# Kernel optimization log

Measured on AMD Instinct MI355X. Metric: run time of the kernel, lower is better.

The kernel has to match this reference:

```python
import jax, jax.numpy as jnp
import numpy as np

NUM_VARI = 32
DIM_PER_VARI = 128  # input feature dim is 2*DIM_PER_VARI
DIM_TO = 256
BATCH = 4096
TWO_D = 2 * DIM_PER_VARI


def setup_inputs() -> dict:
    key = jax.random.key(0)
    k1, k2, k3 = jax.random.split(key, 3)
    x = jax.random.normal(k1, (NUM_VARI, BATCH, TWO_D), dtype=jnp.float32)
    # parameters, initialized like reset_parameters(): U(-std, std), std = 1/sqrt(num_vari)
    std = 1.0 / np.sqrt(NUM_VARI)
    dense_w = jax.random.uniform(k2, (NUM_VARI, 1, TWO_D, DIM_TO), dtype=jnp.float32,
                                 minval=-std, maxval=std)
    dense_bias = jax.random.uniform(k3, (NUM_VARI, 1, 1, DIM_TO), dtype=jnp.float32,
                                    minval=-std, maxval=std)
    return {"x": x, "dense_w": dense_w, "dense_bias": dense_bias}


def reference(x, dense_w, dense_bias):
    # Original: (x.unsqueeze(-1) * W + b).sum(2)
    # = grouped matmul over the feature axis + (2*dim_per_vari) * bias
    # x: [V, B, 2D], W: [V, 1, 2D, O] -> out: [V, B, O]
    out = jnp.einsum('vbd,vdo->vbo', x, dense_w[:, 0])
    out = out + TWO_D * dense_bias[:, 0]  # bias broadcast [V,1,O] -> [V,B,O]
    # activation_type == 'softplus' (original intends F.softplus)
    return jax.nn.softplus(out)
```

## Files before the change

### kernel.cpp

```cpp
#include <hip/hip_runtime.h>
#include <stdint.h>
#include <math.h>

#define NV 32
#define NB 4096
#define NK 256
#define NO 256

#define TROWS 16
#define NTILE 16

typedef __bf16 bf16x8 __attribute__((ext_vector_type(8)));
typedef float  f32x4  __attribute__((ext_vector_type(4)));

__device__ __forceinline__ f32x4 mfma16(bf16x8 a, bf16x8 b, f32x4 c) {
    return __builtin_amdgcn_mfma_f32_16x16x32_bf16(a, b, c, 0, 0, 0);
}

__device__ __forceinline__ float softplus_f(float z) {
    return fmaxf(z, 0.0f) + __logf(1.0f + __expf(-fabsf(z)));
}

__device__ __forceinline__ void gload_lds16(const void* g, void* l) {
    __builtin_amdgcn_global_load_lds((const __attribute__((address_space(1))) uint32_t*)g,
                                     (__attribute__((address_space(3))) uint32_t*)l,
                                     16, 0, 0);
}

__global__ __launch_bounds__(256)
void prep_wt_kernel(const float* __restrict__ w, __bf16* __restrict__ wt) {
    const int id = blockIdx.x * 256 + threadIdx.x;
    const int o  = id & 255;
    const int kc = (id >> 8) & 31;
    const int v  = id >> 13;
    const float* src = w + ((size_t)v * NK + (size_t)kc * 8) * NO + o;
    bf16x8 r;
#pragma unroll
    for (int j = 0; j < 8; ++j) r[j] = (__bf16)src[(size_t)j * NO];
    *(bf16x8*)(wt + ((size_t)v * NO + o) * NK + kc * 8) = r;
}

__global__ __launch_bounds__(512, 4)
void mv_dense_kernel(const float* __restrict__ x, const __bf16* __restrict__ wt,
                     const float* __restrict__ bias, float* __restrict__ out) {
    __shared__ float Xs[3][TROWS][NK];

    const int t    = threadIdx.x;
    const int w    = t >> 6;
    const int lane = t & 63;
    const int lr   = lane & 15;
    const int lg   = lane >> 4;

    const int bid  = blockIdx.x;
    const int lb   = (bid & 7) * 64 + (bid >> 3);
    const int v    = lb >> 4;
    const int slab = lb & 15;

    const float*  xg = x    + ((size_t)v * NB + (size_t)slab * 256) * NK;
    float*        og = out  + ((size_t)v * NB + (size_t)slab * 256) * NO;

    const __bf16* wp0 = wt + ((size_t)v * NO + w * 32 + lr) * NK + lg * 8;
    const __bf16* wp1 = wp0 + (size_t)16 * NK;
    bf16x8 wv0[8], wv1[8];
#pragma unroll
    for (int kk = 0; kk < 8; ++kk) {
        wv0[kk] = *(const bf16x8*)(wp0 + kk * 32);
        wv1[kk] = *(const bf16x8*)(wp1 + kk * 32);
    }

    const float* bg = bias + (size_t)v * NO + w * 32 + lg * 4;
    f32x4 bb0 = *(const f32x4*)bg;
    f32x4 bb1 = *(const f32x4*)(bg + 16);
#pragma unroll
    for (int r = 0; r < 4; ++r) { bb0[r] *= 256.0f; bb1[r] *= 256.0f; }

    const int cl = lane ^ (w & 7);
    auto stage = [&](int tile, int buf) {
        const float* s0 = xg + (size_t)(tile * TROWS + w)     * NK + cl * 4;
        const float* s1 = xg + (size_t)(tile * TROWS + w + 8) * NK + cl * 4;
        gload_lds16(s0, (void*)&Xs[buf][w][0]);
        gload_lds16(s1, (void*)&Xs[buf][w + 8][0]);
    };

    const int b0c   = (2 * lg) ^ (lr & 7);
    const int aoff0 = lr * 1024 + b0c * 16;
    const int aoff1 = lr * 1024 + (b0c ^ 1) * 16;

    auto compute = [&](int tile, int buf) {
        const char* tb = (const char*)&Xs[buf][0][0];
        f32x4 acc0 = {0.f, 0.f, 0.f, 0.f};
        f32x4 acc1 = {0.f, 0.f, 0.f, 0.f};
#pragma unroll
        for (int kk = 0; kk < 8; ++kk) {
            f32x4 lo = *(const f32x4*)(tb + aoff0 + kk * 128);
            f32x4 hi = *(const f32x4*)(tb + aoff1 + kk * 128);
            bf16x8 bf;
#pragma unroll
            for (int e = 0; e < 4; ++e) { bf[e] = (__bf16)lo[e]; bf[e + 4] = (__bf16)hi[e]; }
            acc0 = mfma16(wv0[kk], bf, acc0);
            acc1 = mfma16(wv1[kk], bf, acc1);
        }
        float* o = og + (size_t)(tile * TROWS + lr) * NO + w * 32 + lg * 4;
        f32x4 r0, r1;
#pragma unroll
        for (int r = 0; r < 4; ++r) {
            r0[r] = softplus_f(acc0[r] + bb0[r]);
            r1[r] = softplus_f(acc1[r] + bb1[r]);
        }
        *(f32x4*)o        = r0;
        *(f32x4*)(o + 16) = r1;
    };

    stage(0, 0);
    stage(1, 1);

    asm volatile("s_waitcnt vmcnt(0)" ::: "memory");
    __builtin_amdgcn_s_barrier();
    __builtin_amdgcn_sched_barrier(0);
    stage(2, 2);
    compute(0, 0);

#pragma unroll 1
    for (int tt = 1; tt < NTILE; ++tt) {
        asm volatile("s_waitcnt vmcnt(4)" ::: "memory");
        __builtin_amdgcn_s_barrier();
        __builtin_amdgcn_sched_barrier(0);
        if (tt + 2 < NTILE) stage(tt + 2, (tt + 2) % 3);
        compute(tt, tt % 3);
    }
}

extern "C" void kernel_launch(void* const* d_in, const int* in_sizes, int n_in,
                              void* d_out, int out_size, void* d_ws, size_t ws_size,
                              hipStream_t stream) {
    const float* x  = (const float*)d_in[0];
    const float* w  = (const float*)d_in[1];
    const float* b  = (const float*)d_in[2];
    float* out      = (float*)d_out;
    __bf16* wt      = (__bf16*)d_ws;

    hipLaunchKernelGGL(prep_wt_kernel, dim3(1024), dim3(256), 0, stream, w, wt);
    hipLaunchKernelGGL(mv_dense_kernel, dim3(512), dim3(512), 0, stream,
                       x, wt, b, out);
}
```

Measured before the change: 66.38 us.

## Stage x through registers as bf16 in LDS with larger 64-row tiles

The x tile is no longer copied into LDS as fp32 by direct global-to-LDS loads. Instead it is loaded into registers, converted to bf16, and written into a swizzled, double-buffered LDS tile of 64 rows rather than 16. Each wave now computes four 16-row MFMA blocks per tile, and the weight fragments are re-read from global memory inside the k loop instead of being kept in registers. The aim is to halve LDS footprint and traffic, convert each x element once, and cut the number of barriers. In exchange it adds repeated weight loads, register-staged prefetch and a shallower pipeline.

```diff
diff --git a/kernel.cpp b/kernel.cpp
--- a/kernel.cpp
+++ b/kernel.cpp
@@ -7,10 +7,11 @@
 #define NK 256
 #define NO 256
 
-#define TROWS 16
-#define NTILE 16
+#define TROWS 64
+#define NTILE 4
 
 typedef __bf16 bf16x8 __attribute__((ext_vector_type(8)));
+typedef __bf16 bf16x4 __attribute__((ext_vector_type(4)));
 typedef float  f32x4  __attribute__((ext_vector_type(4)));
 
 __device__ __forceinline__ f32x4 mfma16(bf16x8 a, bf16x8 b, f32x4 c) {
@@ -19,12 +20,6 @@
 
 __device__ __forceinline__ float softplus_f(float z) {
     return fmaxf(z, 0.0f) + __logf(1.0f + __expf(-fabsf(z)));
-}
-
-__device__ __forceinline__ void gload_lds16(const void* g, void* l) {
-    __builtin_amdgcn_global_load_lds((const __attribute__((address_space(1))) uint32_t*)g,
-                                     (__attribute__((address_space(3))) uint32_t*)l,
-                                     16, 0, 0);
 }
 
 __global__ __launch_bounds__(256)
@@ -43,7 +38,7 @@
 __global__ __launch_bounds__(512, 4)
 void mv_dense_kernel(const float* __restrict__ x, const __bf16* __restrict__ wt,
                      const float* __restrict__ bias, float* __restrict__ out) {
-    __shared__ float Xs[3][TROWS][NK];
+    __shared__ __bf16 Xs[2][TROWS * NK];
 
     const int t    = threadIdx.x;
     const int w    = t >> 6;
@@ -56,17 +51,11 @@
     const int v    = lb >> 4;
     const int slab = lb & 15;
 
-    const float*  xg = x    + ((size_t)v * NB + (size_t)slab * 256) * NK;
-    float*        og = out  + ((size_t)v * NB + (size_t)slab * 256) * NO;
+    const float* xg = x   + ((size_t)v * NB + (size_t)slab * 256) * NK;
+    float*       og = out + ((size_t)v * NB + (size_t)slab * 256) * NO;
 
     const __bf16* wp0 = wt + ((size_t)v * NO + w * 32 + lr) * NK + lg * 8;
     const __bf16* wp1 = wp0 + (size_t)16 * NK;
-    bf16x8 wv0[8], wv1[8];
-#pragma unroll
-    for (int kk = 0; kk < 8; ++kk) {
-        wv0[kk] = *(const bf16x8*)(wp0 + kk * 32);
-        wv1[kk] = *(const bf16x8*)(wp1 + kk * 32);
-    }
 
     const float* bg = bias + (size_t)v * NO + w * 32 + lg * 4;
     f32x4 bb0 = *(const f32x4*)bg;
@@ -74,59 +63,81 @@
 #pragma unroll
     for (int r = 0; r < 4; ++r) { bb0[r] *= 256.0f; bb1[r] *= 256.0f; }
 
-    const int cl = lane ^ (w & 7);
-    auto stage = [&](int tile, int buf) {
-        const float* s0 = xg + (size_t)(tile * TROWS + w)     * NK + cl * 4;
-        const float* s1 = xg + (size_t)(tile * TROWS + w + 8) * NK + cl * 4;
-        gload_lds16(s0, (void*)&Xs[buf][w][0]);
-        gload_lds16(s1, (void*)&Xs[buf][w + 8][0]);
+    const float* xsrc = xg + w * NK + lane * 4;
+    const int ldso = w * NK + (((lane >> 1) ^ w) * 8) + (lane & 1) * 4;
+
+    f32x4 xa[8];
+    auto stage_load = [&](int tile) {
+#pragma unroll
+        for (int n = 0; n < 8; ++n)
+            xa[n] = *(const f32x4*)(xsrc + (size_t)tile * TROWS * NK + n * 8 * NK);
+    };
+    auto cvt_write = [&](__bf16* buf) {
+#pragma unroll
+        for (int n = 0; n < 8; ++n) {
+            bf16x4 hv;
+#pragma unroll
+            for (int e = 0; e < 4; ++e) hv[e] = (__bf16)xa[n][e];
+            *(bf16x4*)&buf[n * 8 * NK + ldso] = hv;
+        }
     };
 
-    const int b0c   = (2 * lg) ^ (lr & 7);
-    const int aoff0 = lr * 1024 + b0c * 16;
-    const int aoff1 = lr * 1024 + (b0c ^ 1) * 16;
-
-    auto compute = [&](int tile, int buf) {
-        const char* tb = (const char*)&Xs[buf][0][0];
-        f32x4 acc0 = {0.f, 0.f, 0.f, 0.f};
-        f32x4 acc1 = {0.f, 0.f, 0.f, 0.f};
+    auto compute = [&](int tile, const __bf16* buf) {
+        f32x4 acc[4][2];
+#pragma unroll
+        for (int i = 0; i < 4; ++i)
+#pragma unroll
+            for (int j = 0; j < 2; ++j) {
+                f32x4 z4 = {0.f, 0.f, 0.f, 0.f};
+                acc[i][j] = z4;
+            }
 #pragma unroll
         for (int kk = 0; kk < 8; ++kk) {
-            f32x4 lo = *(const f32x4*)(tb + aoff0 + kk * 128);
-            f32x4 hi = *(const f32x4*)(tb + aoff1 + kk * 128);
-            bf16x8 bf;
+            bf16x8 wv0 = *(const bf16x8*)(wp0 + kk * 32);
+            bf16x8 wv1 = *(const bf16x8*)(wp1 + kk * 32);
 #pragma unroll
-            for (int e = 0; e < 4; ++e) { bf[e] = (__bf16)lo[e]; bf[e + 4] = (__bf16)hi[e]; }
-            acc0 = mfma16(wv0[kk], bf, acc0);
-            acc1 = mfma16(wv1[kk], bf, acc1);
+            for (int i = 0; i < 4; ++i) {
+                const int row  = i * 16 + lr;
+                const int phys = (kk * 4 + lg) ^ (lr & 7);
+                bf16x8 afr = *(const bf16x8*)&buf[row * NK + phys * 8];
+                acc[i][0] = mfma16(wv0, afr, acc[i][0]);
+                acc[i][1] = mfma16(wv1, afr, acc[i][1]);
+            }
         }
-        float* o = og + (size_t)(tile * TROWS + lr) * NO + w * 32 + lg * 4;
-        f32x4 r0, r1;
 #pragma unroll
-        for (int r = 0; r < 4; ++r) {
-            r0[r] = softplus_f(acc0[r] + bb0[r]);
-            r1[r] = softplus_f(acc1[r] + bb1[r]);
+        for (int i = 0; i < 4; ++i) {
+            float* o = og + (size_t)(tile * TROWS + i * 16 + lr) * NO + w * 32 + lg * 4;
+            f32x4 r0, r1;
+#pragma unroll
+            for (int r = 0; r < 4; ++r) {
+                r0[r] = softplus_f(acc[i][0][r] + bb0[r]);
+                r1[r] = softplus_f(acc[i][1][r] + bb1[r]);
+            }
+            *(f32x4*)o        = r0;
+            *(f32x4*)(o + 16) = r1;
         }
-        *(f32x4*)o        = r0;
-        *(f32x4*)(o + 16) = r1;
     };
 
-    stage(0, 0);
-    stage(1, 1);
+    stage_load(0);
+    asm volatile("s_waitcnt vmcnt(0)" ::: "memory");
+    cvt_write(&Xs[0][0]);
+    stage_load(1);
+    __builtin_amdgcn_sched_barrier(0);
+    __builtin_amdgcn_s_barrier();
 
-    asm volatile("s_waitcnt vmcnt(0)" ::: "memory");
-    __builtin_amdgcn_s_barrier();
-    __builtin_amdgcn_sched_barrier(0);
-    stage(2, 2);
-    compute(0, 0);
-
+    __bf16* cur = &Xs[0][0];
+    __bf16* nxt = &Xs[1][0];
 #pragma unroll 1
-    for (int tt = 1; tt < NTILE; ++tt) {
-        asm volatile("s_waitcnt vmcnt(4)" ::: "memory");
-        __builtin_amdgcn_s_barrier();
-        __builtin_amdgcn_sched_barrier(0);
-        if (tt + 2 < NTILE) stage(tt + 2, (tt + 2) % 3);
-        compute(tt, tt % 3);
+    for (int tt = 0; tt < NTILE; ++tt) {
+        compute(tt, cur);
+        if (tt + 1 < NTILE) {
+            asm volatile("s_waitcnt vmcnt(8)" ::: "memory");
+            cvt_write(nxt);
+            if (tt + 2 < NTILE) stage_load(tt + 2);
+            __builtin_amdgcn_sched_barrier(0);
+            __builtin_amdgcn_s_barrier();
+            __bf16* tmp = cur; cur = nxt; nxt = tmp;
+        }
     }
 }
 
```

After: 112.9 us. 70.1% more time.

## Halve rows per block, double grid, and reload weights per tile instead of registers

Applied to the files above, without the earlier changes.

Each block now handles 128 batch rows (8 tiles) instead of 256, and the grid grows to 1024 blocks to spread work over more CUs and waves. The bf16 weight fragments are no longer held in 32 registers across the loop but reloaded from global/L2 inside each k step, which lowers register pressure. Occupancy hint drops from 4 to 3 and the LDS swizzle is rewritten per row. In exchange, weight loads repeat every tile and the shorter per-block pipeline exposes more prologue/epilogue overhead.

```diff
diff --git a/kernel.cpp b/kernel.cpp
--- a/kernel.cpp
+++ b/kernel.cpp
@@ -8,7 +8,7 @@
 #define NO 256
 
 #define TROWS 16
-#define NTILE 16
+#define NTILE 8
 
 typedef __bf16 bf16x8 __attribute__((ext_vector_type(8)));
 typedef float  f32x4  __attribute__((ext_vector_type(4)));
@@ -40,10 +40,10 @@
     *(bf16x8*)(wt + ((size_t)v * NO + o) * NK + kc * 8) = r;
 }
 
-__global__ __launch_bounds__(512, 4)
+__global__ __launch_bounds__(512, 3)
 void mv_dense_kernel(const float* __restrict__ x, const __bf16* __restrict__ wt,
                      const float* __restrict__ bias, float* __restrict__ out) {
-    __shared__ float Xs[3][TROWS][NK];
+    __shared__ float Xs[3][TROWS * NK];
 
     const int t    = threadIdx.x;
     const int w    = t >> 6;
@@ -52,21 +52,15 @@
     const int lg   = lane >> 4;
 
     const int bid  = blockIdx.x;
-    const int lb   = (bid & 7) * 64 + (bid >> 3);
-    const int v    = lb >> 4;
-    const int slab = lb & 15;
+    const int lb   = (bid & 7) * 128 + (bid >> 3);
+    const int v    = lb >> 5;
+    const int slab = lb & 31;
 
-    const float*  xg = x    + ((size_t)v * NB + (size_t)slab * 256) * NK;
-    float*        og = out  + ((size_t)v * NB + (size_t)slab * 256) * NO;
+    const float* xg = x   + ((size_t)v * NB + (size_t)slab * 128) * NK;
+    float*       og = out + ((size_t)v * NB + (size_t)slab * 128) * NO;
 
     const __bf16* wp0 = wt + ((size_t)v * NO + w * 32 + lr) * NK + lg * 8;
     const __bf16* wp1 = wp0 + (size_t)16 * NK;
-    bf16x8 wv0[8], wv1[8];
-#pragma unroll
-    for (int kk = 0; kk < 8; ++kk) {
-        wv0[kk] = *(const bf16x8*)(wp0 + kk * 32);
-        wv1[kk] = *(const bf16x8*)(wp1 + kk * 32);
-    }
 
     const float* bg = bias + (size_t)v * NO + w * 32 + lg * 4;
     f32x4 bb0 = *(const f32x4*)bg;
@@ -74,33 +68,35 @@
 #pragma unroll
     for (int r = 0; r < 4; ++r) { bb0[r] *= 256.0f; bb1[r] *= 256.0f; }
 
-    const int cl = lane ^ (w & 7);
     auto stage = [&](int tile, int buf) {
-        const float* s0 = xg + (size_t)(tile * TROWS + w)     * NK + cl * 4;
-        const float* s1 = xg + (size_t)(tile * TROWS + w + 8) * NK + cl * 4;
-        gload_lds16(s0, (void*)&Xs[buf][w][0]);
-        gload_lds16(s1, (void*)&Xs[buf][w + 8][0]);
+        const float* tsrc = xg + (size_t)tile * TROWS * NK;
+        char* lbase = (char*)&Xs[buf][0];
+#pragma unroll
+        for (int d = 0; d < 2; ++d) {
+            const int r = d * 8 + w;
+            gload_lds16(tsrc + (size_t)r * NK + (lane ^ r) * 4,
+                        (void*)(lbase + (size_t)r * 1024));
+        }
     };
 
-    const int b0c   = (2 * lg) ^ (lr & 7);
-    const int aoff0 = lr * 1024 + b0c * 16;
-    const int aoff1 = lr * 1024 + (b0c ^ 1) * 16;
-
-    auto compute = [&](int tile, int buf) {
-        const char* tb = (const char*)&Xs[buf][0][0];
+    auto compute = [&](int tt, const char* tb) {
         f32x4 acc0 = {0.f, 0.f, 0.f, 0.f};
         f32x4 acc1 = {0.f, 0.f, 0.f, 0.f};
 #pragma unroll
         for (int kk = 0; kk < 8; ++kk) {
-            f32x4 lo = *(const f32x4*)(tb + aoff0 + kk * 128);
-            f32x4 hi = *(const f32x4*)(tb + aoff1 + kk * 128);
-            bf16x8 bf;
+            bf16x8 wv0 = *(const bf16x8*)(wp0 + kk * 32);
+            bf16x8 wv1 = *(const bf16x8*)(wp1 + kk * 32);
+            const int phys = (kk * 8 + lg * 2) ^ lr;
+            const char* rb = tb + (size_t)lr * 1024;
+            f32x4 lo = *(const f32x4*)(rb + phys * 16);
+            f32x4 hi = *(const f32x4*)(rb + (phys ^ 1) * 16);
+            bf16x8 a;
 #pragma unroll
-            for (int e = 0; e < 4; ++e) { bf[e] = (__bf16)lo[e]; bf[e + 4] = (__bf16)hi[e]; }
-            acc0 = mfma16(wv0[kk], bf, acc0);
-            acc1 = mfma16(wv1[kk], bf, acc1);
+            for (int e = 0; e < 4; ++e) { a[e] = (__bf16)lo[e]; a[e + 4] = (__bf16)hi[e]; }
+            acc0 = mfma16(wv0, a, acc0);
+            acc1 = mfma16(wv1, a, acc1);
         }
-        float* o = og + (size_t)(tile * TROWS + lr) * NO + w * 32 + lg * 4;
+        float* o = og + (size_t)(tt * TROWS + lr) * NO + w * 32 + lg * 4;
         f32x4 r0, r1;
 #pragma unroll
         for (int r = 0; r < 4; ++r) {
@@ -113,12 +109,11 @@
 
     stage(0, 0);
     stage(1, 1);
-
     asm volatile("s_waitcnt vmcnt(0)" ::: "memory");
     __builtin_amdgcn_s_barrier();
     __builtin_amdgcn_sched_barrier(0);
     stage(2, 2);
-    compute(0, 0);
+    compute(0, (const char*)&Xs[0][0]);
 
 #pragma unroll 1
     for (int tt = 1; tt < NTILE; ++tt) {
@@ -126,7 +121,7 @@
         __builtin_amdgcn_s_barrier();
         __builtin_amdgcn_sched_barrier(0);
         if (tt + 2 < NTILE) stage(tt + 2, (tt + 2) % 3);
-        compute(tt, tt % 3);
+        compute(tt, (const char*)&Xs[tt % 3][0]);
     }
 }
 
@@ -140,6 +135,6 @@
     __bf16* wt      = (__bf16*)d_ws;
 
     hipLaunchKernelGGL(prep_wt_kernel, dim3(1024), dim3(256), 0, stream, w, wt);
-    hipLaunchKernelGGL(mv_dense_kernel, dim3(512), dim3(512), 0, stream,
+    hipLaunchKernelGGL(mv_dense_kernel, dim3(NV * 32), dim3(512), 0, stream,
                        x, wt, b, out);
 }
```

Measured after the change: 76.92 us. +15.9%, slower.
